# Kernel tuning notes

Hardware: AMD Instinct MI355X
Metric: run time of the kernel (lower is better)

The kernel has to match this reference:

```python
import jax, jax.numpy as jnp
import numpy as np

N = 50000       # nodes
E = 800000      # edges (before self-loops)
NFEAT = 256
NHID = 16       # per-head hidden dim
HEADS = 8
NCLASS = 16
NEG_SLOPE = 0.2  # PyG GATConv default leaky-relu slope


def setup_inputs() -> dict:
    key = jax.random.key(0)
    ks = jax.random.split(key, 10)
    s = 0.05  # weight scale for numerical sanity
    return {
        "x": jax.random.normal(ks[0], (N, NFEAT), jnp.float32),
        "edge_index": jax.random.randint(ks[1], (2, E), 0, N, dtype=jnp.int32),
        "W1": jax.random.normal(ks[2], (NFEAT, HEADS * NHID), jnp.float32) * s,
        "att_src1": jax.random.normal(ks[3], (HEADS, NHID), jnp.float32) * s,
        "att_dst1": jax.random.normal(ks[4], (HEADS, NHID), jnp.float32) * s,
        "b1": jnp.zeros((HEADS * NHID,), jnp.float32),
        "W2": jax.random.normal(ks[5], (HEADS * NHID, NCLASS), jnp.float32) * s,
        "att_src2": jax.random.normal(ks[6], (1, NCLASS), jnp.float32) * s,
        "att_dst2": jax.random.normal(ks[7], (1, NCLASS), jnp.float32) * s,
        "b2": jnp.zeros((NCLASS,), jnp.float32),
    }


def gat_conv(x, edge_index, W, a_src, a_dst, b, heads, out_c, concat):
    """Faithful PyG GATConv (eval mode: dropout off, add_self_loops=True)."""
    n = x.shape[0]
    loop = jnp.arange(n, dtype=edge_index.dtype)
    src = jnp.concatenate([edge_index[0], loop])  # [E+N]
    dst = jnp.concatenate([edge_index[1], loop])  # [E+N]
    h = (x @ W).reshape(n, heads, out_c)          # [N, H, C]
    # per-node attention logits
    alpha_src = jnp.einsum('nhc,hc->nh', h, a_src)  # [N, H]
    alpha_dst = jnp.einsum('nhc,hc->nh', h, a_dst)  # [N, H]
    e = jax.nn.leaky_relu(alpha_src[src] + alpha_dst[dst], NEG_SLOPE)  # [E+N, H]
    # segment softmax over incoming edges of each dst node (self-loop guarantees nonempty)
    m = jax.lax.stop_gradient(jax.ops.segment_max(e, dst, num_segments=n))
    p = jnp.exp(e - m[dst])
    denom = jax.ops.segment_sum(p, dst, num_segments=n)
    a = p / denom[dst]                              # [E+N, H]
    out = jax.ops.segment_sum(a[:, :, None] * h[src], dst, num_segments=n)  # [N, H, C]
    out = out.reshape(n, heads * out_c) if concat else out.mean(axis=1)
    return out + b


def reference(x, edge_index, W1, att_src1, att_dst1, b1, W2, att_src2, att_dst2, b2):
    h1 = jax.nn.elu(gat_conv(x, edge_index, W1, att_src1, att_dst1, b1, HEADS, NHID, True))
    return gat_conv(h1, edge_index, W2, att_src2, att_dst2, b2, 1, NCLASS, False)
```

## Files before the change

kernel.cpp:

```cpp
#include <hip/hip_runtime.h>
#include <hip/hip_bf16.h>

#define NNODES 50000
#define NEDGES 800000
#define NFEATS 256
#define NHID 16
#define HEADS 8
#define NCLS 16
#define NEG_SLOPE 0.2f
#define TOTE (NEDGES + NNODES)
#define RSTRIDE 64
#define NBUCK 196
#define NPB 256
#define BCAP 4864
#define S1_EPT 16
#define BIN_BLOCKS ((TOTE + 4095) / 4096)
#define GSTRIDE 16
#define GEMM1_BLOCKS ((NNODES + 127) / 128)

typedef __attribute__((ext_vector_type(8))) short short8;
typedef __attribute__((ext_vector_type(4))) float floatx4;

static __device__ __forceinline__ short f2bf(float f) {
    __hip_bfloat16 b = __float2bfloat16(f);
    return *reinterpret_cast<short*>(&b);
}

#define AS1 __attribute__((address_space(1)))
#define AS3 __attribute__((address_space(3)))

static __device__ __forceinline__ void ld_lds16(const void* g, void* l) {
#if __has_builtin(__builtin_amdgcn_global_load_lds)
    __builtin_amdgcn_global_load_lds((const AS1 void*)g, (AS3 void*)l, 16, 0, 0);
#endif
}


__global__ __launch_bounds__(256) void k_bin(const int* __restrict__ ei,
                                             int* __restrict__ gcnt, int* __restrict__ barr,
                                             const float* __restrict__ W,
                                             const float* __restrict__ a_s,
                                             const float* __restrict__ a_d,
                                             short* __restrict__ Wsw) {
    int tid = threadIdx.x;
    if (blockIdx.x >= BIN_BLOCKS) {
        int t = (blockIdx.x - BIN_BLOCKS) * 256 + tid;
        if (t >= 4608) return;
        short8 b;
        if (t < 4096) {
            int kc = t >> 9, nt = (t >> 6) & 7, lane = t & 63;
            int quad = lane >> 4, lo = lane & 15;
#pragma unroll
            for (int j = 0; j < 8; j++)
                b[j] = f2bf(W[(size_t)(kc * 32 + quad * 8 + j) * 128 + nt * 16 + lo]);
        } else {
            int t2 = t - 4096;
            int kc = t2 >> 6, lane = t2 & 63;
            int quad = lane >> 4, lo = lane & 15;
            int h = lo & 7;
            const float* av = (lo < 8) ? (a_s + h * 16) : (a_d + h * 16);
#pragma unroll
            for (int j = 0; j < 8; j++) {
                int k = kc * 32 + quad * 8 + j;
                float acc = 0.f;
#pragma unroll
                for (int c = 0; c < 16; c++) acc += W[(size_t)k * 128 + h * 16 + c] * av[c];
                b[j] = f2bf(acc);
            }
        }
        *(short8*)(Wsw + (size_t)t * 8) = b;
        return;
    }

    __shared__ int lcnt[NBUCK], lbase[NBUCK];
    if (tid < NBUCK) lcnt[tid] = 0;
    __syncthreads();
    int e0 = blockIdx.x * (256 * S1_EPT) + tid;
    int s[S1_EPT], d[S1_EPT], rk[S1_EPT];
#pragma unroll
    for (int k = 0; k < S1_EPT; k++) {
        int e = e0 + k * 256;
        bool v = e < TOTE;
        int ss = 0, dd = 0;
        if (v) {
            if (e < NEDGES) { ss = ei[e]; dd = ei[NEDGES + e]; }
            else            { ss = e - NEDGES; dd = ss; }
        }
        s[k] = ss; d[k] = dd;
        rk[k] = v ? atomicAdd(&lcnt[dd >> 8], 1) : -1;
    }
    __syncthreads();
    if (tid < NBUCK) lbase[tid] = lcnt[tid] ? atomicAdd(&gcnt[tid * GSTRIDE], lcnt[tid]) : 0;
    __syncthreads();
#pragma unroll
    for (int k = 0; k < S1_EPT; k++) {
        if (rk[k] >= 0) {
            int b = d[k] >> 8;
            int pos = lbase[b] + rk[k];
            if (pos < BCAP)
                barr[(size_t)b * BCAP + pos] = ((d[k] & 255) << 16) | s[k];
        }
    }
}


__global__ __launch_bounds__(256) void k_mid(const int* __restrict__ gcnt,
                                             const int* __restrict__ barr,
                                             int* __restrict__ cnt, int* __restrict__ csr,
                                             const float* __restrict__ x,
                                             const short* __restrict__ Wsw,
                                             __hip_bfloat16* __restrict__ h1,
                                             float* __restrict__ as1, float* __restrict__ ad1) {
    __shared__ short smem[32768];
    int tid = threadIdx.x;

    if (blockIdx.x < NBUCK) {
        int* lcnt = (int*)smem;
        unsigned short* lcsr = (unsigned short*)smem + 512;
        int b = blockIdx.x;
        lcnt[tid] = 0;
        __syncthreads();
        int n = min(gcnt[b * GSTRIDE], BCAP);
        int nodeBase = b << 8;
        for (int i = tid; i < n; i += 256) {
            int e = barr[(size_t)b * BCAP + i];
            int ln = e >> 16;
            int r = atomicAdd(&lcnt[ln], 1);
            if (r < RSTRIDE) lcsr[ln * 65 + r] = (unsigned short)(e & 0xFFFF);
        }
        __syncthreads();
        int node = nodeBase + tid;
        if (node < NNODES) cnt[node] = min(lcnt[tid], RSTRIDE);
        for (int i = tid; i < NPB * RSTRIDE; i += 256) {
            int ln = i >> 6;
            int nn = nodeBase + ln;
            if (nn < NNODES && (i & 63) < min(lcnt[ln], RSTRIDE))
                csr[(size_t)nodeBase * RSTRIDE + i] = (int)lcsr[ln * 65 + (i & 63)];
        }
        return;
    }

    short* bsw = smem;
    int bid  = blockIdx.x - NBUCK;
    int wave = tid >> 6;
    int lane = tid & 63;
    int quad = lane >> 4;
    int lo   = lane & 15;

#if __has_builtin(__builtin_amdgcn_global_load_lds)
    {
        const char* gsrc = (const char*)Wsw + (size_t)wave * 1024 + (size_t)lane * 16;
        char* ldst = (char*)bsw + wave * 1024;
#pragma unroll
        for (int it = 0; it < 16; it++)
            ld_lds16(gsrc + it * 4096, ldst + it * 4096);
    }
#else
    {
        const uint4* g4 = (const uint4*)Wsw;
        uint4* l4 = (uint4*)bsw;
#pragma unroll
        for (int it = 0; it < 16; it++) l4[it * 256 + tid] = g4[it * 256 + tid];
    }
#endif
    short8 wafr[8];
#pragma unroll
    for (int kc = 0; kc < 8; kc++)
        wafr[kc] = *(const short8*)(Wsw + (size_t)(4096 + kc * 64 + lane) * 8);
    __syncthreads();

    int rowBase = bid * 128 + wave * 32;
    const float* xa[2];
#pragma unroll
    for (int mt = 0; mt < 2; mt++) {
        int row = rowBase + mt * 16 + lo;
        row = (row < NNODES) ? row : (NNODES - 1);
        xa[mt] = x + (size_t)row * 256 + quad * 8;
    }

    floatx4 acc[2][8], accA[2];
#pragma unroll
    for (int mt = 0; mt < 2; mt++) {
        accA[mt] = (floatx4){0.f, 0.f, 0.f, 0.f};
#pragma unroll
        for (int nt = 0; nt < 8; nt++) acc[mt][nt] = (floatx4){0.f, 0.f, 0.f, 0.f};
    }

    float4 a0[2], a1[2];
#pragma unroll
    for (int mt = 0; mt < 2; mt++) {
        a0[mt] = *(const float4*)(xa[mt]);
        a1[mt] = *(const float4*)(xa[mt] + 4);
    }

    for (int kc = 0; kc < 8; kc++) {
        float4 n0[2], n1[2];
        if (kc < 7) {
#pragma unroll
            for (int mt = 0; mt < 2; mt++) {
                n0[mt] = *(const float4*)(xa[mt] + (kc + 1) * 32);
                n1[mt] = *(const float4*)(xa[mt] + (kc + 1) * 32 + 4);
            }
        }
        short8 afr[2];
#pragma unroll
        for (int mt = 0; mt < 2; mt++) {
            union { short8 s; __hip_bfloat162 h[4]; } u;
            u.h[0] = __float22bfloat162_rn(make_float2(a0[mt].x, a0[mt].y));
            u.h[1] = __float22bfloat162_rn(make_float2(a0[mt].z, a0[mt].w));
            u.h[2] = __float22bfloat162_rn(make_float2(a1[mt].x, a1[mt].y));
            u.h[3] = __float22bfloat162_rn(make_float2(a1[mt].z, a1[mt].w));
            afr[mt] = u.s;
        }
#pragma unroll
        for (int nt = 0; nt < 8; nt++) {
            short8 bfr = *(const short8*)&bsw[((kc * 8 + nt) * 64 + lane) * 8];
            acc[0][nt] = __builtin_amdgcn_mfma_f32_16x16x32_bf16(afr[0], bfr, acc[0][nt], 0, 0, 0);
            acc[1][nt] = __builtin_amdgcn_mfma_f32_16x16x32_bf16(afr[1], bfr, acc[1][nt], 0, 0, 0);
        }
        accA[0] = __builtin_amdgcn_mfma_f32_16x16x32_bf16(afr[0], wafr[kc], accA[0], 0, 0, 0);
        accA[1] = __builtin_amdgcn_mfma_f32_16x16x32_bf16(afr[1], wafr[kc], accA[1], 0, 0, 0);
#pragma unroll
        for (int mt = 0; mt < 2; mt++) { a0[mt] = n0[mt]; a1[mt] = n1[mt]; }
    }

#pragma unroll
    for (int mt = 0; mt < 2; mt++)
#pragma unroll
        for (int nt = 0; nt < 8; nt++)
#pragma unroll
            for (int reg = 0; reg < 4; reg++) {
                int row = rowBase + mt * 16 + quad * 4 + reg;
                int col = nt * 16 + lo;
                if (row < NNODES)
                    h1[(size_t)row * 128 + col] = __float2bfloat16(acc[mt][nt][reg]);
            }
#pragma unroll
    for (int mt = 0; mt < 2; mt++)
#pragma unroll
        for (int reg = 0; reg < 4; reg++) {
            int row = rowBase + mt * 16 + quad * 4 + reg;
            if (row < NNODES) {
                float v = accA[mt][reg];
                if (lo < 8) as1[(size_t)row * 8 + lo] = v;
                else        ad1[(size_t)row * 8 + (lo - 8)] = v;
            }
        }
}


__global__ __launch_bounds__(256) void k_aggA(const int* __restrict__ cnt, const int* __restrict__ csr,
                                              const __hip_bfloat16* __restrict__ h1,
                                              const float* __restrict__ as1, const float* __restrict__ ad1,
                                              const float* __restrict__ b1,
                                              const float* __restrict__ W2,
                                              const float* __restrict__ a_s2,
                                              const float* __restrict__ a_d2,
                                              float* __restrict__ h2,
                                              float* __restrict__ as2, float* __restrict__ ad2) {
    __shared__ float w2s[2048];
    int tid  = threadIdx.x;
#pragma unroll
    for (int i = 0; i < 8; i++) w2s[i * 256 + tid] = W2[i * 256 + tid];
    __syncthreads();

    int node = blockIdx.x * 4 + (tid >> 6);
    int lane = tid & 63;
    int cl   = lane & 15;
    int slot = lane >> 4;
    int head = cl >> 1;
    int deg  = min(cnt[node], RSTRIDE);
    float adst = ad1[node * 8 + head];
    int rowv = csr[node * RSTRIDE + lane];

    float acc[8] = {0.f, 0.f, 0.f, 0.f, 0.f, 0.f, 0.f, 0.f};
    float s = 0.f;
    for (int i2 = 0; i2 < deg; i2 += 16) {
        float p[4];
        union { short8 v; __hip_bfloat162 h[4]; } u[4];
#pragma unroll
        for (int t = 0; t < 4; t++) {
            int ii = i2 + slot + t * 4;
            int src = __shfl(rowv, ii & 63);
            p[t] = 0.f;
            u[t].v = (short8){0, 0, 0, 0, 0, 0, 0, 0};
            if (ii < deg) {
                u[t].v = *(const short8*)(h1 + (size_t)src * 128 + cl * 8);
                float e = as1[src * 8 + head] + adst;
                e = (e > 0.f) ? e : NEG_SLOPE * e;
                p[t] = __expf(e);
            }
        }
        s += (p[0] + p[1]) + (p[2] + p[3]);
#pragma unroll
        for (int t = 0; t < 4; t++)
#pragma unroll
            for (int q = 0; q < 4; q++) {
                float2 f = __bfloat1622float2(u[t].h[q]);
                acc[q * 2]     = fmaf(p[t], f.x, acc[q * 2]);
                acc[q * 2 + 1] = fmaf(p[t], f.y, acc[q * 2 + 1]);
            }
    }

#pragma unroll
    for (int q = 0; q < 8; q++) {
        acc[q] += __shfl_xor(acc[q], 16);
        acc[q] += __shfl_xor(acc[q], 32);
    }
    s += __shfl_xor(s, 16);
    s += __shfl_xor(s, 32);

    float is = 1.f / s;
    float4 b1a = *(const float4*)(b1 + cl * 8);
    float4 b1b = *(const float4*)(b1 + cl * 8 + 4);
    float v[8];
    v[0] = acc[0] * is + b1a.x; v[1] = acc[1] * is + b1a.y;
    v[2] = acc[2] * is + b1a.z; v[3] = acc[3] * is + b1a.w;
    v[4] = acc[4] * is + b1b.x; v[5] = acc[5] * is + b1b.y;
    v[6] = acc[6] * is + b1b.z; v[7] = acc[7] * is + b1b.w;
#pragma unroll
    for (int q = 0; q < 8; q++) v[q] = (v[q] > 0.f) ? v[q] : (__expf(v[q]) - 1.f);

    float4 part = make_float4(0.f, 0.f, 0.f, 0.f);
#pragma unroll
    for (int q = 0; q < 8; q++) {
        float4 wrow = *(const float4*)(&w2s[(cl * 8 + q) * 16 + slot * 4]);
        part.x = fmaf(v[q], wrow.x, part.x);
        part.y = fmaf(v[q], wrow.y, part.y);
        part.z = fmaf(v[q], wrow.z, part.z);
        part.w = fmaf(v[q], wrow.w, part.w);
    }
#pragma unroll
    for (int o = 1; o <= 8; o <<= 1) {
        part.x += __shfl_xor(part.x, o);
        part.y += __shfl_xor(part.y, o);
        part.z += __shfl_xor(part.z, o);
        part.w += __shfl_xor(part.w, o);
    }
    if (cl == 0) *(float4*)(h2 + (size_t)node * 16 + slot * 4) = part;

    float4 asv = *(const float4*)(a_s2 + slot * 4);
    float4 adv = *(const float4*)(a_d2 + slot * 4);
    float sv = part.x * asv.x + part.y * asv.y + part.z * asv.z + part.w * asv.w;
    float dv = part.x * adv.x + part.y * adv.y + part.z * adv.z + part.w * adv.w;
    sv += __shfl_xor(sv, 16); sv += __shfl_xor(sv, 32);
    dv += __shfl_xor(dv, 16); dv += __shfl_xor(dv, 32);
    if (lane == 0) { as2[node] = sv; ad2[node] = dv; }
}


__global__ __launch_bounds__(256) void k_agg2(const int* __restrict__ cnt, const int* __restrict__ csr,
                                              const float* __restrict__ h2, const float* __restrict__ as2,
                                              const float* __restrict__ ad2, const float* __restrict__ b2,
                                              float* __restrict__ out) {
    int node = blockIdx.x * 4 + (threadIdx.x >> 6);
    int lane = threadIdx.x & 63;
    int c4   = lane & 3;
    int slot = lane >> 2;
    int deg  = min(cnt[node], RSTRIDE);
    float adst = ad2[node];
    int rowv = csr[node * RSTRIDE + lane];

    float4 acc = make_float4(0.f, 0.f, 0.f, 0.f);
    float s = 0.f;
    for (int i2 = 0; i2 < deg; i2 += 32) {
        int ia = i2 + slot;
        int ib = ia + 16;
        int sa = __shfl(rowv, ia & 63);
        int sb = __shfl(rowv, ib & 63);
        float p0 = 0.f, p1 = 0.f;
        float4 r0 = make_float4(0.f, 0.f, 0.f, 0.f);
        float4 r1 = make_float4(0.f, 0.f, 0.f, 0.f);
        if (ia < deg) {
            r0 = *(const float4*)(h2 + (size_t)sa * 16 + c4 * 4);
            float e = as2[sa] + adst;
            e = (e > 0.f) ? e : NEG_SLOPE * e;
            p0 = __expf(e);
        }
        if (ib < deg) {
            r1 = *(const float4*)(h2 + (size_t)sb * 16 + c4 * 4);
            float e = as2[sb] + adst;
            e = (e > 0.f) ? e : NEG_SLOPE * e;
            p1 = __expf(e);
        }
        s += p0 + p1;
        acc.x = fmaf(p0, r0.x, fmaf(p1, r1.x, acc.x));
        acc.y = fmaf(p0, r0.y, fmaf(p1, r1.y, acc.y));
        acc.z = fmaf(p0, r0.z, fmaf(p1, r1.z, acc.z));
        acc.w = fmaf(p0, r0.w, fmaf(p1, r1.w, acc.w));
    }
#pragma unroll
    for (int o = 4; o <= 32; o <<= 1) {
        acc.x += __shfl_xor(acc.x, o);
        acc.y += __shfl_xor(acc.y, o);
        acc.z += __shfl_xor(acc.z, o);
        acc.w += __shfl_xor(acc.w, o);
        s += __shfl_xor(s, o);
    }
    if (slot == 0) {
        float is = 1.f / s;
        float4 o4;
        o4.x = acc.x * is + b2[c4 * 4 + 0];
        o4.y = acc.y * is + b2[c4 * 4 + 1];
        o4.z = acc.z * is + b2[c4 * 4 + 2];
        o4.w = acc.w * is + b2[c4 * 4 + 3];
        *(float4*)(out + (size_t)node * 16 + c4 * 4) = o4;
    }
}


extern "C" void kernel_launch(void* const* d_in, const int* in_sizes, int n_in,
                              void* d_out, int out_size, void* d_ws, size_t ws_size,
                              hipStream_t stream) {
    const float* x    = (const float*)d_in[0];
    const int*   ei   = (const int*)d_in[1];
    const float* W1   = (const float*)d_in[2];
    const float* a_s1 = (const float*)d_in[3];
    const float* a_d1 = (const float*)d_in[4];
    const float* b1   = (const float*)d_in[5];
    const float* W2   = (const float*)d_in[6];
    const float* a_s2 = (const float*)d_in[7];
    const float* a_d2 = (const float*)d_in[8];
    const float* b2   = (const float*)d_in[9];
    float* out = (float*)d_out;

    char* p = (char*)d_ws;
    auto alloc = [&](size_t bytes) -> char* {
        char* q = p;
        p += (bytes + 255) & ~(size_t)255;
        return q;
    };
    int*  gcnt = (int*)alloc((size_t)NBUCK * GSTRIDE * 4);
    int*  barr = (int*)alloc((size_t)NBUCK * BCAP * 4);
    int*  cnt  = (int*)alloc((size_t)NNODES * 4);
    int*  csr  = (int*)alloc((size_t)NNODES * RSTRIDE * 4);
    short* Wsw = (short*)alloc((size_t)36864 * 2);
    __hip_bfloat16* h1 = (__hip_bfloat16*)alloc((size_t)NNODES * 128 * 2);
    float* as1 = (float*)alloc((size_t)NNODES * 8 * 4);
    float* ad1 = (float*)alloc((size_t)NNODES * 8 * 4);
    float* h2  = (float*)alloc((size_t)NNODES * 16 * 4);
    float* as2 = (float*)barr;
    float* ad2 = (float*)barr + NNODES;

    hipMemsetAsync(gcnt, 0, (size_t)NBUCK * GSTRIDE * 4, stream);
    hipLaunchKernelGGL(k_bin,   dim3(BIN_BLOCKS + 18), dim3(256), 0, stream,
                       ei, gcnt, barr, W1, a_s1, a_d1, Wsw);
    hipLaunchKernelGGL(k_mid,   dim3(NBUCK + GEMM1_BLOCKS), dim3(256), 0, stream,
                       gcnt, barr, cnt, csr, x, Wsw, h1, as1, ad1);
    hipLaunchKernelGGL(k_aggA,  dim3(NNODES / 4), dim3(256), 0, stream,
                       cnt, csr, h1, as1, ad1, b1, W2, a_s2, a_d2, h2, as2, ad2);
    hipLaunchKernelGGL(k_agg2,  dim3(NNODES / 4), dim3(256), 0, stream, cnt, csr, h2, as2, ad2, b2, out);
}
```

Measured before the change: 210.7 us.

## Store CSR indices as 16-bit and restructure W2 projection with padded LDS

The padded CSR neighbour array now holds unsigned 16-bit source indices instead of 32-bit ints. Node ids stay below 65536, so this halves the bytes written by k_mid and read by both aggregation kernels. The layer-2 projection in k_aggA is also rewritten: W2 goes into LDS with a 17-float row pitch to avoid bank conflicts, and each lane computes one output class through 32 shuffle-and-FMA steps instead of float4 partial sums plus a butterfly reduction. That trades strided float4 LDS reads, which likely conflicted, for more cross-lane shuffles, and it only works while node ids fit in 16 bits.

```diff
diff --git a/kernel.cpp b/kernel.cpp
--- a/kernel.cpp
+++ b/kernel.cpp
@@ -106,7 +106,7 @@
 
 __global__ __launch_bounds__(256) void k_mid(const int* __restrict__ gcnt,
                                              const int* __restrict__ barr,
-                                             int* __restrict__ cnt, int* __restrict__ csr,
+                                             int* __restrict__ cnt, unsigned short* __restrict__ csr,
                                              const float* __restrict__ x,
                                              const short* __restrict__ Wsw,
                                              __hip_bfloat16* __restrict__ h1,
@@ -135,7 +135,7 @@
             int ln = i >> 6;
             int nn = nodeBase + ln;
             if (nn < NNODES && (i & 63) < min(lcnt[ln], RSTRIDE))
-                csr[(size_t)nodeBase * RSTRIDE + i] = (int)lcsr[ln * 65 + (i & 63)];
+                csr[(size_t)nodeBase * RSTRIDE + i] = lcsr[ln * 65 + (i & 63)];
         }
         return;
     }
@@ -249,7 +249,8 @@
 }
 
 
-__global__ __launch_bounds__(256) void k_aggA(const int* __restrict__ cnt, const int* __restrict__ csr,
+__global__ __launch_bounds__(256) void k_aggA(const int* __restrict__ cnt,
+                                              const unsigned short* __restrict__ csr,
                                               const __hip_bfloat16* __restrict__ h1,
                                               const float* __restrict__ as1, const float* __restrict__ ad1,
                                               const float* __restrict__ b1,
@@ -258,10 +259,13 @@
                                               const float* __restrict__ a_d2,
                                               float* __restrict__ h2,
                                               float* __restrict__ as2, float* __restrict__ ad2) {
-    __shared__ float w2s[2048];
+    __shared__ float w2s[2176];
     int tid  = threadIdx.x;
 #pragma unroll
-    for (int i = 0; i < 8; i++) w2s[i * 256 + tid] = W2[i * 256 + tid];
+    for (int i = 0; i < 8; i++) {
+        int e = i * 256 + tid;
+        w2s[(e >> 4) * 17 + (e & 15)] = W2[e];
+    }
     __syncthreads();
 
     int node = blockIdx.x * 4 + (tid >> 6);
@@ -321,35 +325,30 @@
 #pragma unroll
     for (int q = 0; q < 8; q++) v[q] = (v[q] > 0.f) ? v[q] : (__expf(v[q]) - 1.f);
 
-    float4 part = make_float4(0.f, 0.f, 0.f, 0.f);
-#pragma unroll
-    for (int q = 0; q < 8; q++) {
-        float4 wrow = *(const float4*)(&w2s[(cl * 8 + q) * 16 + slot * 4]);
-        part.x = fmaf(v[q], wrow.x, part.x);
-        part.y = fmaf(v[q], wrow.y, part.y);
-        part.z = fmaf(v[q], wrow.z, part.z);
-        part.w = fmaf(v[q], wrow.w, part.w);
-    }
+    float outp = 0.f;
+#pragma unroll
+    for (int j = 0; j < 32; j++) {
+        float vk = __shfl(v[j & 7], slot * 4 + (j >> 3));
+        float wk = w2s[(slot * 32 + j) * 17 + cl];
+        outp = fmaf(vk, wk, outp);
+    }
+    outp += __shfl_xor(outp, 16);
+    outp += __shfl_xor(outp, 32);
+    if (slot == 0) h2[(size_t)node * 16 + cl] = outp;
+
+    float sv = outp * a_s2[cl];
+    float dv = outp * a_d2[cl];
 #pragma unroll
     for (int o = 1; o <= 8; o <<= 1) {
-        part.x += __shfl_xor(part.x, o);
-        part.y += __shfl_xor(part.y, o);
-        part.z += __shfl_xor(part.z, o);
-        part.w += __shfl_xor(part.w, o);
-    }
-    if (cl == 0) *(float4*)(h2 + (size_t)node * 16 + slot * 4) = part;
-
-    float4 asv = *(const float4*)(a_s2 + slot * 4);
-    float4 adv = *(const float4*)(a_d2 + slot * 4);
-    float sv = part.x * asv.x + part.y * asv.y + part.z * asv.z + part.w * asv.w;
-    float dv = part.x * adv.x + part.y * adv.y + part.z * adv.z + part.w * adv.w;
-    sv += __shfl_xor(sv, 16); sv += __shfl_xor(sv, 32);
-    dv += __shfl_xor(dv, 16); dv += __shfl_xor(dv, 32);
+        sv += __shfl_xor(sv, o);
+        dv += __shfl_xor(dv, o);
+    }
     if (lane == 0) { as2[node] = sv; ad2[node] = dv; }
 }
 
 
-__global__ __launch_bounds__(256) void k_agg2(const int* __restrict__ cnt, const int* __restrict__ csr,
+__global__ __launch_bounds__(256) void k_agg2(const int* __restrict__ cnt,
+                                              const unsigned short* __restrict__ csr,
                                               const float* __restrict__ h2, const float* __restrict__ as2,
                                               const float* __restrict__ ad2, const float* __restrict__ b2,
                                               float* __restrict__ out) {
@@ -433,7 +432,7 @@
     int*  gcnt = (int*)alloc((size_t)NBUCK * GSTRIDE * 4);
     int*  barr = (int*)alloc((size_t)NBUCK * BCAP * 4);
     int*  cnt  = (int*)alloc((size_t)NNODES * 4);
-    int*  csr  = (int*)alloc((size_t)NNODES * RSTRIDE * 4);
+    unsigned short* csr = (unsigned short*)alloc((size_t)NNODES * RSTRIDE * 2);
     short* Wsw = (short*)alloc((size_t)36864 * 2);
     __hip_bfloat16* h1 = (__hip_bfloat16*)alloc((size_t)NNODES * 128 * 2);
     float* as1 = (float*)alloc((size_t)NNODES * 8 * 4);
```

Result: no change. 208.6 us (-1.0%).
